# Kernel optimization log

Hardware: AMD Instinct MI355X
Metric: run time of the kernel (lower is better)

The kernel has to match this reference:

```python
import jax, jax.numpy as jnp
import numpy as np
import math

D_MODEL = 1024
NHEAD = 16
D_K = D_MODEL // NHEAD
SEQ = 2048
BATCH = 2


def setup_inputs() -> dict:
    key = jax.random.key(0)
    ks = jax.random.split(key, 8)
    s = 1.0 / math.sqrt(D_MODEL)
    return {
        "q": jax.random.normal(ks[0], (SEQ, BATCH, D_MODEL), jnp.float32),
        "k": jax.random.normal(ks[1], (SEQ, BATCH, D_MODEL), jnp.float32),
        "v": jax.random.normal(ks[2], (SEQ, BATCH, D_MODEL), jnp.float32),
        "mask": jnp.zeros((1, 1, SEQ, SEQ), jnp.float32),
        "Wq": jax.random.normal(ks[3], (D_MODEL, D_MODEL), jnp.float32) * s,
        "bq": jnp.zeros((D_MODEL,), jnp.float32),
        "Wk": jax.random.normal(ks[4], (D_MODEL, D_MODEL), jnp.float32) * s,
        "bk": jnp.zeros((D_MODEL,), jnp.float32),
        "Wv": jax.random.normal(ks[5], (D_MODEL, D_MODEL), jnp.float32) * s,
        "bv": jnp.zeros((D_MODEL,), jnp.float32),
        "Wo": jax.random.normal(ks[6], (D_MODEL, D_MODEL), jnp.float32) * s,
        "bo": jnp.zeros((D_MODEL,), jnp.float32),
    }


def _split_heads(x):
    # (seq, batch, d_model) -> (batch, nhead, seq, d_k)
    S, B, _ = x.shape
    return x.reshape(S, B, NHEAD, D_K).transpose(1, 2, 0, 3)


def reference(q, k, v, mask, Wq, bq, Wk, bk, Wv, bv, Wo, bo):
    S, B, _ = q.shape
    qh = _split_heads(q @ Wq.T + bq)  # (B, H, S, Dk)
    kh = _split_heads(k @ Wk.T + bk)
    vh = _split_heads(v @ Wv.T + bv)
    scale = 1.0 / math.sqrt(D_K)
    scores = jnp.einsum("bhsd,bhtd->bhst", qh, kh) * scale + mask
    attn = jax.nn.softmax(scores, axis=-1)  # dropout is identity at inference
    out = jnp.einsum("bhst,bhtd->bhsd", attn, vh)  # (B, H, S, Dk)
    # combine heads -> (S, B, d_model), then output projection
    out = out.transpose(2, 0, 1, 3).reshape(S, B, D_MODEL)
    return out @ Wo.T + bo
```

## Files before the change

kernel.cpp:

```cpp
#include <hip/hip_runtime.h>


#define DEV static __device__ __forceinline__

typedef unsigned short u16;
typedef __attribute__((ext_vector_type(8))) short short8;
typedef __attribute__((ext_vector_type(4))) float f32x4;
typedef __attribute__((ext_vector_type(16))) float f32x16;
typedef __attribute__((ext_vector_type(4))) unsigned short ushort4v;
typedef __attribute__((ext_vector_type(4))) unsigned int uint4v;

#define SEQ   2048
#define BATCH 2
#define DM    1024
#define NH    16
#define DKH   64
#define MROWS (SEQ*BATCH)

DEV u16 f2bf(float f) {
  union { float f; unsigned int u; } v; v.f = f;
  unsigned int u = v.u;
  return (u16)((u + 0x7FFFu + ((u >> 16) & 1u)) >> 16);
}

DEV unsigned int cvtpk_bf16(float lo, float hi) {
  unsigned int r;
  asm("v_cvt_pk_bf16_f32 %0, %1, %2" : "=v"(r) : "v"(lo), "v"(hi));
  return r;
}

DEV void permswap(unsigned int& a, unsigned int& b) {
  asm volatile("v_permlane32_swap_b32 %0, %1" : "+v"(a), "+v"(b));
}

#if __has_builtin(__builtin_amdgcn_exp2f)
#define EXP2(x) __builtin_amdgcn_exp2f(x)
#else
#define EXP2(x) exp2f(x)
#endif

DEV void async16(const void* g, void* l) {
  __builtin_amdgcn_global_load_lds(
      (const __attribute__((address_space(1))) unsigned int*)g,
      (__attribute__((address_space(3))) unsigned int*)l, 16, 0, 0);
}

struct CvtArgs {
  const float* s[8];
  u16* d[8];
  int n[8];
  float scale[8];
  int* flag;
};

__global__ __launch_bounds__(256) void cvt_kernel(CvtArgs a) {
  const int t = blockIdx.y;
  const int n = a.n[t];
  const int stride = 1024 * 256 * 4;
  if (t == 7) {
    const float* __restrict__ m = a.s[7];
    int any = 0;
    for (int i = (blockIdx.x * 256 + threadIdx.x) * 4; i < n; i += stride) {
      f32x4 v = *(const f32x4*)&m[i];
      any |= (v[0] != 0.f); any |= (v[1] != 0.f);
      any |= (v[2] != 0.f); any |= (v[3] != 0.f);
    }
    if (any) atomicOr(a.flag, 1);
    return;
  }
  const float* __restrict__ s = a.s[t];
  u16* __restrict__ d = a.d[t];
  const float sc = a.scale[t];
  for (int i = (blockIdx.x * 256 + threadIdx.x) * 4; i < n; i += stride) {
    f32x4 f = *(const f32x4*)&s[i];
    ushort4v o;
    o[0] = f2bf(f[0] * sc); o[1] = f2bf(f[1] * sc);
    o[2] = f2bf(f[2] * sc); o[3] = f2bf(f[3] * sc);
    *(ushort4v*)&d[i] = o;
  }
}

template <int MT, int NT, typename OutT>
DEV void gemm_body(const u16* __restrict__ A,
                   const u16* __restrict__ W,
                   const float* __restrict__ bias, float bscale,
                   OutT* __restrict__ C,
                   u16* As, u16* Bs,
                   int M, int N, int K, int m0, int n0) {
  const int tid = threadIdx.x;
  const int lane = tid & 63;
  const int wid = tid >> 6;
  const int wr = wid >> 1, wc = wid & 1;
  const int sr = lane & 15, g = lane >> 4;

  f32x4 acc[MT][NT] = {};

  const int arow = tid >> 3;
  const int acol = (tid & 7) * 8;
  const size_t abase = (size_t)(m0 + arow) * K + acol;
  const size_t bbase = (size_t)(n0 + arow) * K + acol;

  for (int kt = 0; kt < K; kt += 64) {
#pragma unroll
    for (int j = 0; j < MT; ++j)
      async16(A + abase + (size_t)j * 32 * K + kt, (char*)As + j * 4096 + wid * 1024);
#pragma unroll
    for (int j = 0; j < NT; ++j)
      async16(W + bbase + (size_t)j * 32 * K + kt, (char*)Bs + j * 4096 + wid * 1024);
    __syncthreads();
#pragma unroll
    for (int kk = 0; kk < 2; ++kk) {
      short8 af[MT], bf[NT];
#pragma unroll
      for (int mt = 0; mt < MT; ++mt)
        af[mt] = *(const short8*)&As[(wr * MT * 16 + mt * 16 + sr) * 64 + kk * 32 + g * 8];
#pragma unroll
      for (int nt = 0; nt < NT; ++nt)
        bf[nt] = *(const short8*)&Bs[(wc * NT * 16 + nt * 16 + sr) * 64 + kk * 32 + g * 8];
#pragma unroll
      for (int mt = 0; mt < MT; ++mt)
#pragma unroll
        for (int nt = 0; nt < NT; ++nt)
          acc[mt][nt] = __builtin_amdgcn_mfma_f32_16x16x32_bf16(af[mt], bf[nt], acc[mt][nt], 0, 0, 0);
    }
    __syncthreads();
  }

#pragma unroll
  for (int nt = 0; nt < NT; ++nt) {
    const int col = n0 + wc * NT * 16 + nt * 16 + sr;
    const float bv = bias[col] * bscale;
#pragma unroll
    for (int mt = 0; mt < MT; ++mt) {
#pragma unroll
      for (int r = 0; r < 4; ++r) {
        const int row = m0 + wr * MT * 16 + mt * 16 + g * 4 + r;
        const float val = acc[mt][nt][r] + bv;
        if constexpr (sizeof(OutT) == 2)
          C[(size_t)row * N + col] = f2bf(val);
        else
          C[(size_t)row * N + col] = val;
      }
    }
  }
}

struct GemmPtrs {
  const u16* A[3];
  const u16* W[3];
  const float* bias[3];
  float bscale[3];
  u16* C[3];
};

__global__ __launch_bounds__(256) void gemm_qkv_kernel(GemmPtrs p, int M, int N, int K) {
  __shared__ u16 As[64 * 64];
  __shared__ u16 Bs[128 * 64];
  const int z = blockIdx.z;
  const int fl = blockIdx.x + 64 * blockIdx.y;
  const int virt = (fl & 7) * 64 + (fl >> 3);
  const int mb = virt >> 3, nb = virt & 7;
  gemm_body<2, 4, u16>(p.A[z], p.W[z], p.bias[z], p.bscale[z], p.C[z], As, Bs,
                       M, N, K, mb * 64, nb * 128);
}

__global__ __launch_bounds__(256) void gemm_f32_kernel(const u16* __restrict__ A,
                                                       const u16* __restrict__ W,
                                                       const float* __restrict__ bias,
                                                       float* __restrict__ C,
                                                       int M, int N, int K) {
  __shared__ u16 As[64 * 64];
  __shared__ u16 Bs[128 * 64];
  const int fl = blockIdx.x + 64 * blockIdx.y;
  const int virt = (fl & 7) * 64 + (fl >> 3);
  const int mb = virt >> 3, nb = virt & 7;
  gemm_body<2, 4, float>(A, W, bias, 1.0f, C, As, Bs, M, N, K,
                         mb * 64, nb * 128);
}

__global__ __launch_bounds__(256) void vtrans_kernel(const u16* __restrict__ Vh,
                                                     u16* __restrict__ VT) {
  __shared__ u16 tl[4096];
  const int tid = threadIdx.x;
  const int w = tid >> 6;
  const int t0 = blockIdx.x * 64;
  const int bh = blockIdx.y;
  const int b = bh >> 4, h = bh & 15;
  const int str = tid >> 3;
  const int scc = (tid & 7) * 8;
#pragma unroll
  for (int it = 0; it < 2; ++it)
    async16(Vh + (size_t)((t0 + str + it * 32) * 2 + b) * 1024 + h * 64 + scc,
            (char*)tl + it * 4096 + w * 1024);
  __syncthreads();
  const int dk = tid >> 2;
  const int t4 = (tid & 3) * 16;
  short8 ov[2];
#pragma unroll
  for (int half = 0; half < 2; ++half)
#pragma unroll
    for (int j = 0; j < 8; ++j)
      ov[half][j] = (short)tl[(t4 + half * 8 + j) * 64 + dk];
  u16* dst = VT + (size_t)(bh * 64 + dk) * 2048 + t0 + t4;
  *(short8*)dst = ov[0];
  *(short8*)(dst + 8) = ov[1];
}

__global__ __launch_bounds__(256, 2) void attn8_kernel(const u16* __restrict__ Q,
                                                       const u16* __restrict__ K,
                                                       const u16* __restrict__ VT,
                                                       const float* __restrict__ mask,
                                                       const int* __restrict__ maskflag,
                                                       u16* __restrict__ O) {
  __shared__ u16 Kl[2][2][4096];
  __shared__ u16 Vl[2][2][4096];

  const int tid = threadIdx.x;
  const int lane = tid & 63;
  const int w = tid >> 6;
  const int ln = lane & 31;
  const int hi = lane >> 5;
  const int sw = (ln & 7) << 4;

  const int flat = blockIdx.x;
  const int virt = ((flat & 7) << 6) | (flat >> 3);
  const int qi = virt & 15;
  const int bh = virt >> 4;
  const int q0 = qi * 128 + w * 32;
  const int b = bh >> 4, h = bh & 15;
  const int usemask = *maskflag;

  const u16* Qb = Q + b * DM + h * DKH;
  const u16* Kb = K + b * DM + h * DKH;
  const u16* VTb = VT + (size_t)bh * 64 * 2048;

  short8 aq[4];
#pragma unroll
  for (int ks = 0; ks < 4; ++ks)
    aq[ks] = *(const short8*)&Qb[(size_t)(q0 + ln) * 2048 + ks * 16 + hi * 8];

  f32x16 acc[2] = {};
  float l_ = 0.f;
  const float L2E = 1.44269504088896f;

  const int strow = tid >> 3;
  const int scb = (((tid & 7) * 16) ^ ((strow & 7) << 4)) >> 1;

  auto STAGE = [&](int nb, int t0n) {
#pragma unroll
    for (int st = 0; st < 2; ++st)
#pragma unroll
      for (int it = 0; it < 2; ++it) {
        async16(Kb + (size_t)(t0n + st * 64 + strow + it * 32) * 2048 + scb,
                (char*)&Kl[nb][st][0] + it * 4096 + w * 1024);
        async16(VTb + (size_t)(strow + it * 32) * 2048 + t0n + st * 64 + scb,
                (char*)&Vl[nb][st][0] + it * 4096 + w * 1024);
      }
  };

  STAGE(0, 0);
  __syncthreads();
  int cur = 0;

  for (int tp = 0; tp < SEQ; tp += 128) {
    if (tp + 128 < SEQ) STAGE(cur ^ 1, tp + 128);

#pragma unroll
    for (int st = 0; st < 2; ++st) {
      const int t0 = tp + st * 64;

      short8 kf[2][4];
#pragma unroll
      for (int tb = 0; tb < 2; ++tb)
#pragma unroll
        for (int ks = 0; ks < 4; ++ks)
          kf[tb][ks] = *(const short8*)((const char*)&Kl[cur][st][0] +
                                        (tb * 32 + ln) * 128 + ((ks * 32 + hi * 16) ^ sw));

      f32x16 sc[2] = {};
      __builtin_amdgcn_s_setprio(1);
#pragma unroll
      for (int tb = 0; tb < 2; ++tb)
#pragma unroll
        for (int ks = 0; ks < 4; ++ks)
          sc[tb] = __builtin_amdgcn_mfma_f32_32x32x16_bf16(kf[tb][ks], aq[ks], sc[tb], 0, 0, 0);
      __builtin_amdgcn_s_setprio(0);

      short8 vf[2][4];
#pragma unroll
      for (int db = 0; db < 2; ++db)
#pragma unroll
        for (int ks = 0; ks < 4; ++ks)
          vf[db][ks] = *(const short8*)((const char*)&Vl[cur][st][0] +
                                        (db * 32 + ln) * 128 + ((ks * 32 + hi * 16) ^ sw));

      short8 pa[4];
      float rs = 0.f;
#pragma unroll
      for (int tb = 0; tb < 2; ++tb) {
        float p[16];
#pragma unroll
        for (int r = 0; r < 16; ++r) {
          float xv = sc[tb][r];
          if (usemask)
            xv = __builtin_fmaf(
                mask[(size_t)(q0 + ln) * SEQ + t0 + tb * 32 + (r & 3) + 8 * (r >> 2) + 4 * hi],
                L2E, xv);
          p[r] = EXP2(xv);
          rs += p[r];
        }
#pragma unroll
        for (int ksl = 0; ksl < 2; ++ksl) {
          unsigned int c0 = cvtpk_bf16(p[8 * ksl + 0], p[8 * ksl + 1]);
          unsigned int c1 = cvtpk_bf16(p[8 * ksl + 2], p[8 * ksl + 3]);
          unsigned int c4 = cvtpk_bf16(p[8 * ksl + 4], p[8 * ksl + 5]);
          unsigned int c5 = cvtpk_bf16(p[8 * ksl + 6], p[8 * ksl + 7]);
          permswap(c0, c4);
          permswap(c1, c5);
          union { uint4v u; short8 s; } cc;
          cc.u[0] = c0; cc.u[1] = c1; cc.u[2] = c4; cc.u[3] = c5;
          pa[tb * 2 + ksl] = cc.s;
        }
      }
      l_ += rs;

      __builtin_amdgcn_s_setprio(1);
#pragma unroll
      for (int ks = 0; ks < 4; ++ks)
#pragma unroll
        for (int db = 0; db < 2; ++db)
          acc[db] = __builtin_amdgcn_mfma_f32_32x32x16_bf16(pa[ks], vf[db][ks], acc[db], 0, 0, 0);
      __builtin_amdgcn_s_setprio(0);
    }

    __syncthreads();
    cur ^= 1;
  }

  l_ += __shfl_xor(l_, 32);
  const float linv = 1.f / l_;
  float lb[16];
#pragma unroll
  for (int r = 0; r < 16; ++r)
    lb[r] = __shfl(linv, (r & 3) + 8 * (r >> 2) + 4 * hi);
  const size_t obase = (size_t)b * DM + h * DKH;
#pragma unroll
  for (int db = 0; db < 2; ++db)
#pragma unroll
    for (int r = 0; r < 16; ++r) {
      const int q = q0 + (r & 3) + 8 * (r >> 2) + 4 * hi;
      O[(size_t)q * 2048 + obase + db * 32 + ln] = f2bf(acc[db][r] * lb[r]);
    }
}

extern "C" void kernel_launch(void* const* d_in, const int* in_sizes, int n_in,
                              void* d_out, int out_size, void* d_ws, size_t ws_size,
                              hipStream_t stream) {
  const float* q = (const float*)d_in[0];
  const float* k = (const float*)d_in[1];
  const float* v = (const float*)d_in[2];
  const float* msk = (const float*)d_in[3];
  const float* Wq = (const float*)d_in[4];
  const float* bq = (const float*)d_in[5];
  const float* Wk = (const float*)d_in[6];
  const float* bk = (const float*)d_in[7];
  const float* Wv = (const float*)d_in[8];
  const float* bv = (const float*)d_in[9];
  const float* Wo = (const float*)d_in[10];
  const float* bo = (const float*)d_in[11];
  float* out = (float*)d_out;

  char* ws = (char*)d_ws;
  const size_t SZX = (size_t)MROWS * DM * 2;
  const size_t SZW = (size_t)DM * DM * 2;
  u16* qb  = (u16*)(ws + 0 * SZX);
  u16* kb  = (u16*)(ws + 1 * SZX);
  u16* vb  = (u16*)(ws + 2 * SZX);
  u16* Wqb = (u16*)(ws + 3 * SZX + 0 * SZW);
  u16* Wkb = (u16*)(ws + 3 * SZX + 1 * SZW);
  u16* Wvb = (u16*)(ws + 3 * SZX + 2 * SZW);
  u16* Wob = (u16*)(ws + 3 * SZX + 3 * SZW);
  u16* Qh  = (u16*)(ws + 3 * SZX + 4 * SZW + 0 * SZX);
  u16* Kh  = (u16*)(ws + 3 * SZX + 4 * SZW + 1 * SZX);
  u16* Vh  = (u16*)(ws + 3 * SZX + 4 * SZW + 2 * SZX);
  u16* AO  = (u16*)(ws + 3 * SZX + 4 * SZW + 3 * SZX);
  int* flag = (int*)(ws + 7 * SZX + 4 * SZW);
  u16* VTg = qb;

  hipMemsetAsync(flag, 0, 4, stream);

  const float QS = 0.125f * 1.44269504088896f;

  CvtArgs ca;
  ca.s[0] = q;  ca.d[0] = qb;  ca.n[0] = MROWS * DM; ca.scale[0] = 1.f;
  ca.s[1] = k;  ca.d[1] = kb;  ca.n[1] = MROWS * DM; ca.scale[1] = 1.f;
  ca.s[2] = v;  ca.d[2] = vb;  ca.n[2] = MROWS * DM; ca.scale[2] = 1.f;
  ca.s[3] = Wq; ca.d[3] = Wqb; ca.n[3] = DM * DM;    ca.scale[3] = QS;
  ca.s[4] = Wk; ca.d[4] = Wkb; ca.n[4] = DM * DM;    ca.scale[4] = 1.f;
  ca.s[5] = Wv; ca.d[5] = Wvb; ca.n[5] = DM * DM;    ca.scale[5] = 1.f;
  ca.s[6] = Wo; ca.d[6] = Wob; ca.n[6] = DM * DM;    ca.scale[6] = 1.f;
  ca.s[7] = msk; ca.d[7] = nullptr; ca.n[7] = SEQ * SEQ; ca.scale[7] = 1.f;
  ca.flag = flag;
  cvt_kernel<<<dim3(1024, 8, 1), 256, 0, stream>>>(ca);

  GemmPtrs gp;
  gp.A[0] = qb; gp.W[0] = Wqb; gp.bias[0] = bq; gp.bscale[0] = QS;  gp.C[0] = Qh;
  gp.A[1] = kb; gp.W[1] = Wkb; gp.bias[1] = bk; gp.bscale[1] = 1.f; gp.C[1] = Kh;
  gp.A[2] = vb; gp.W[2] = Wvb; gp.bias[2] = bv; gp.bscale[2] = 1.f; gp.C[2] = Vh;
  gemm_qkv_kernel<<<dim3(64, 8, 3), 256, 0, stream>>>(gp, MROWS, DM, DM);

  vtrans_kernel<<<dim3(32, 32, 1), 256, 0, stream>>>(Vh, VTg);

  attn8_kernel<<<dim3(512, 1, 1), 256, 0, stream>>>(Qh, Kh, VTg, msk, flag, AO);

  gemm_f32_kernel<<<dim3(64, 8, 1), 256, 0, stream>>>(AO, Wob, bo, out, MROWS, DM, DM);
}
```

Before: 147.4 us.

## Fuse fp32-to-bf16 activation conversion into QKV GEMM and retile output GEMM

The QKV projection now loads the fp32 q/k/v activations straight into shared memory and converts them to bf16 while building the MFMA fragments. This removes the separate conversion pass over the three activation tensors and its bf16 round trip through memory. The cost is twice the shared-memory footprint and global traffic for the A tile, plus conversion ALU work that is repeated in every N-block. The output projection GEMM also moves to 64x64 tiles with twice as many blocks, trading per-block reuse for more parallelism.

```diff
diff --git a/kernel.cpp b/kernel.cpp
--- a/kernel.cpp
+++ b/kernel.cpp
@@ -57,8 +57,8 @@
   const int t = blockIdx.y;
   const int n = a.n[t];
   const int stride = 1024 * 256 * 4;
-  if (t == 7) {
-    const float* __restrict__ m = a.s[7];
+  if (a.d[t] == nullptr) {
+    const float* __restrict__ m = a.s[t];
     int any = 0;
     for (int i = (blockIdx.x * 256 + threadIdx.x) * 4; i < n; i += stride) {
       f32x4 v = *(const f32x4*)&m[i];
@@ -80,88 +80,90 @@
   }
 }
 
-template <int MT, int NT, typename OutT>
-DEV void gemm_body(const u16* __restrict__ A,
-                   const u16* __restrict__ W,
-                   const float* __restrict__ bias, float bscale,
-                   OutT* __restrict__ C,
-                   u16* As, u16* Bs,
-                   int M, int N, int K, int m0, int n0) {
+struct QkvArgs {
+  const float* A[3];
+  const u16* W[3];
+  const float* bias[3];
+  float bscale[3];
+  u16* C[3];
+};
+
+__global__ __launch_bounds__(256) void gemm_qkvf_kernel(QkvArgs p, int M, int N, int K) {
+  __shared__ float Asf[64 * 64];
+  __shared__ u16 Bs[128 * 64];
+  const int z = blockIdx.z;
+  const float* __restrict__ A = p.A[z];
+  const u16* __restrict__ W = p.W[z];
+  const int fl = blockIdx.x + 64 * blockIdx.y;
+  const int virt = (fl & 7) * 64 + (fl >> 3);
+  const int mb = virt >> 3, nb = virt & 7;
+  const int m0 = mb * 64, n0 = nb * 128;
+
   const int tid = threadIdx.x;
   const int lane = tid & 63;
   const int wid = tid >> 6;
   const int wr = wid >> 1, wc = wid & 1;
   const int sr = lane & 15, g = lane >> 4;
 
-  f32x4 acc[MT][NT] = {};
-
-  const int arow = tid >> 3;
-  const int acol = (tid & 7) * 8;
-  const size_t abase = (size_t)(m0 + arow) * K + acol;
-  const size_t bbase = (size_t)(n0 + arow) * K + acol;
+  f32x4 acc[2][4] = {};
+
+  const int arow_a = tid >> 4;
+  const int acol_a = (tid & 15) * 4;
+  const int arow_b = tid >> 3;
+  const int acol_b = (tid & 7) * 8;
 
   for (int kt = 0; kt < K; kt += 64) {
 #pragma unroll
-    for (int j = 0; j < MT; ++j)
-      async16(A + abase + (size_t)j * 32 * K + kt, (char*)As + j * 4096 + wid * 1024);
-#pragma unroll
-    for (int j = 0; j < NT; ++j)
-      async16(W + bbase + (size_t)j * 32 * K + kt, (char*)Bs + j * 4096 + wid * 1024);
+    for (int it = 0; it < 4; ++it)
+      async16(A + (size_t)(m0 + it * 16 + arow_a) * K + kt + acol_a,
+              (char*)Asf + it * 4096 + wid * 1024);
+#pragma unroll
+    for (int j = 0; j < 4; ++j)
+      async16(W + (size_t)(n0 + j * 32 + arow_b) * K + kt + acol_b,
+              (char*)Bs + j * 4096 + wid * 1024);
     __syncthreads();
 #pragma unroll
     for (int kk = 0; kk < 2; ++kk) {
-      short8 af[MT], bf[NT];
-#pragma unroll
-      for (int mt = 0; mt < MT; ++mt)
-        af[mt] = *(const short8*)&As[(wr * MT * 16 + mt * 16 + sr) * 64 + kk * 32 + g * 8];
-#pragma unroll
-      for (int nt = 0; nt < NT; ++nt)
-        bf[nt] = *(const short8*)&Bs[(wc * NT * 16 + nt * 16 + sr) * 64 + kk * 32 + g * 8];
-#pragma unroll
-      for (int mt = 0; mt < MT; ++mt)
-#pragma unroll
-        for (int nt = 0; nt < NT; ++nt)
+      short8 af[2], bf[4];
+#pragma unroll
+      for (int mt = 0; mt < 2; ++mt) {
+        const float* ap = &Asf[(wr * 32 + mt * 16 + sr) * 64 + kk * 32 + g * 8];
+        f32x4 a0 = *(const f32x4*)ap;
+        f32x4 a1 = *(const f32x4*)(ap + 4);
+        union { uint4v u; short8 s; } ca_;
+        ca_.u[0] = cvtpk_bf16(a0[0], a0[1]);
+        ca_.u[1] = cvtpk_bf16(a0[2], a0[3]);
+        ca_.u[2] = cvtpk_bf16(a1[0], a1[1]);
+        ca_.u[3] = cvtpk_bf16(a1[2], a1[3]);
+        af[mt] = ca_.s;
+      }
+#pragma unroll
+      for (int nt = 0; nt < 4; ++nt)
+        bf[nt] = *(const short8*)&Bs[(wc * 64 + nt * 16 + sr) * 64 + kk * 32 + g * 8];
+#pragma unroll
+      for (int mt = 0; mt < 2; ++mt)
+#pragma unroll
+        for (int nt = 0; nt < 4; ++nt)
           acc[mt][nt] = __builtin_amdgcn_mfma_f32_16x16x32_bf16(af[mt], bf[nt], acc[mt][nt], 0, 0, 0);
     }
     __syncthreads();
   }
 
-#pragma unroll
-  for (int nt = 0; nt < NT; ++nt) {
-    const int col = n0 + wc * NT * 16 + nt * 16 + sr;
+  const float* __restrict__ bias = p.bias[z];
+  const float bscale = p.bscale[z];
+  u16* __restrict__ C = p.C[z];
+#pragma unroll
+  for (int nt = 0; nt < 4; ++nt) {
+    const int col = n0 + wc * 64 + nt * 16 + sr;
     const float bv = bias[col] * bscale;
 #pragma unroll
-    for (int mt = 0; mt < MT; ++mt) {
+    for (int mt = 0; mt < 2; ++mt)
 #pragma unroll
       for (int r = 0; r < 4; ++r) {
-        const int row = m0 + wr * MT * 16 + mt * 16 + g * 4 + r;
-        const float val = acc[mt][nt][r] + bv;
-        if constexpr (sizeof(OutT) == 2)
-          C[(size_t)row * N + col] = f2bf(val);
-        else
-          C[(size_t)row * N + col] = val;
+        const int row = m0 + wr * 32 + mt * 16 + g * 4 + r;
+        C[(size_t)row * N + col] = f2bf(acc[mt][nt][r] + bv);
       }
-    }
-  }
-}
-
-struct GemmPtrs {
-  const u16* A[3];
-  const u16* W[3];
-  const float* bias[3];
-  float bscale[3];
-  u16* C[3];
-};
-
-__global__ __launch_bounds__(256) void gemm_qkv_kernel(GemmPtrs p, int M, int N, int K) {
-  __shared__ u16 As[64 * 64];
-  __shared__ u16 Bs[128 * 64];
-  const int z = blockIdx.z;
-  const int fl = blockIdx.x + 64 * blockIdx.y;
-  const int virt = (fl & 7) * 64 + (fl >> 3);
-  const int mb = virt >> 3, nb = virt & 7;
-  gemm_body<2, 4, u16>(p.A[z], p.W[z], p.bias[z], p.bscale[z], p.C[z], As, Bs,
-                       M, N, K, mb * 64, nb * 128);
+  }
 }
 
 __global__ __launch_bounds__(256) void gemm_f32_kernel(const u16* __restrict__ A,
@@ -170,12 +172,62 @@
                                                        float* __restrict__ C,
                                                        int M, int N, int K) {
   __shared__ u16 As[64 * 64];
-  __shared__ u16 Bs[128 * 64];
+  __shared__ u16 Bs[64 * 64];
   const int fl = blockIdx.x + 64 * blockIdx.y;
-  const int virt = (fl & 7) * 64 + (fl >> 3);
-  const int mb = virt >> 3, nb = virt & 7;
-  gemm_body<2, 4, float>(A, W, bias, 1.0f, C, As, Bs, M, N, K,
-                         mb * 64, nb * 128);
+  const int virt = (fl & 7) * 128 + (fl >> 3);
+  const int mb = virt >> 4, nb = virt & 15;
+  const int m0 = mb * 64, n0 = nb * 64;
+
+  const int tid = threadIdx.x;
+  const int lane = tid & 63;
+  const int wid = tid >> 6;
+  const int wr = wid >> 1, wc = wid & 1;
+  const int sr = lane & 15, g = lane >> 4;
+
+  f32x4 acc[2][2] = {};
+
+  const int arow = tid >> 3;
+  const int acol = (tid & 7) * 8;
+  const size_t abase = (size_t)(m0 + arow) * K + acol;
+  const size_t bbase = (size_t)(n0 + arow) * K + acol;
+
+  for (int kt = 0; kt < K; kt += 64) {
+#pragma unroll
+    for (int j = 0; j < 2; ++j) {
+      async16(A + abase + (size_t)j * 32 * K + kt, (char*)As + j * 4096 + wid * 1024);
+      async16(W + bbase + (size_t)j * 32 * K + kt, (char*)Bs + j * 4096 + wid * 1024);
+    }
+    __syncthreads();
+#pragma unroll
+    for (int kk = 0; kk < 2; ++kk) {
+      short8 af[2], bf[2];
+#pragma unroll
+      for (int mt = 0; mt < 2; ++mt)
+        af[mt] = *(const short8*)&As[(wr * 32 + mt * 16 + sr) * 64 + kk * 32 + g * 8];
+#pragma unroll
+      for (int nt = 0; nt < 2; ++nt)
+        bf[nt] = *(const short8*)&Bs[(wc * 32 + nt * 16 + sr) * 64 + kk * 32 + g * 8];
+#pragma unroll
+      for (int mt = 0; mt < 2; ++mt)
+#pragma unroll
+        for (int nt = 0; nt < 2; ++nt)
+          acc[mt][nt] = __builtin_amdgcn_mfma_f32_16x16x32_bf16(af[mt], bf[nt], acc[mt][nt], 0, 0, 0);
+    }
+    __syncthreads();
+  }
+
+#pragma unroll
+  for (int nt = 0; nt < 2; ++nt) {
+    const int col = n0 + wc * 32 + nt * 16 + sr;
+    const float bv = bias[col];
+#pragma unroll
+    for (int mt = 0; mt < 2; ++mt)
+#pragma unroll
+      for (int r = 0; r < 4; ++r) {
+        const int row = m0 + wr * 32 + mt * 16 + g * 4 + r;
+        C[(size_t)row * N + col] = acc[mt][nt][r] + bv;
+      }
+  }
 }
 
 __global__ __launch_bounds__(256) void vtrans_kernel(const u16* __restrict__ Vh,
@@ -373,9 +425,6 @@
   char* ws = (char*)d_ws;
   const size_t SZX = (size_t)MROWS * DM * 2;
   const size_t SZW = (size_t)DM * DM * 2;
-  u16* qb  = (u16*)(ws + 0 * SZX);
-  u16* kb  = (u16*)(ws + 1 * SZX);
-  u16* vb  = (u16*)(ws + 2 * SZX);
   u16* Wqb = (u16*)(ws + 3 * SZX + 0 * SZW);
   u16* Wkb = (u16*)(ws + 3 * SZX + 1 * SZW);
   u16* Wvb = (u16*)(ws + 3 * SZX + 2 * SZW);
@@ -385,33 +434,30 @@
   u16* Vh  = (u16*)(ws + 3 * SZX + 4 * SZW + 2 * SZX);
   u16* AO  = (u16*)(ws + 3 * SZX + 4 * SZW + 3 * SZX);
   int* flag = (int*)(ws + 7 * SZX + 4 * SZW);
-  u16* VTg = qb;
+  u16* VTg = (u16*)(ws + 0 * SZX);
 
   hipMemsetAsync(flag, 0, 4, stream);
 
   const float QS = 0.125f * 1.44269504088896f;
 
-  CvtArgs ca;
-  ca.s[0] = q;  ca.d[0] = qb;  ca.n[0] = MROWS * DM; ca.scale[0] = 1.f;
-  ca.s[1] = k;  ca.d[1] = kb;  ca.n[1] = MROWS * DM; ca.scale[1] = 1.f;
-  ca.s[2] = v;  ca.d[2] = vb;  ca.n[2] = MROWS * DM; ca.scale[2] = 1.f;
-  ca.s[3] = Wq; ca.d[3] = Wqb; ca.n[3] = DM * DM;    ca.scale[3] = QS;
-  ca.s[4] = Wk; ca.d[4] = Wkb; ca.n[4] = DM * DM;    ca.scale[4] = 1.f;
-  ca.s[5] = Wv; ca.d[5] = Wvb; ca.n[5] = DM * DM;    ca.scale[5] = 1.f;
-  ca.s[6] = Wo; ca.d[6] = Wob; ca.n[6] = DM * DM;    ca.scale[6] = 1.f;
-  ca.s[7] = msk; ca.d[7] = nullptr; ca.n[7] = SEQ * SEQ; ca.scale[7] = 1.f;
+  CvtArgs ca = {};
+  ca.s[0] = Wq; ca.d[0] = Wqb; ca.n[0] = DM * DM;    ca.scale[0] = QS;
+  ca.s[1] = Wk; ca.d[1] = Wkb; ca.n[1] = DM * DM;    ca.scale[1] = 1.f;
+  ca.s[2] = Wv; ca.d[2] = Wvb; ca.n[2] = DM * DM;    ca.scale[2] = 1.f;
+  ca.s[3] = Wo; ca.d[3] = Wob; ca.n[3] = DM * DM;    ca.scale[3] = 1.f;
+  ca.s[4] = msk; ca.d[4] = nullptr; ca.n[4] = SEQ * SEQ; ca.scale[4] = 1.f;
   ca.flag = flag;
-  cvt_kernel<<<dim3(1024, 8, 1), 256, 0, stream>>>(ca);
-
-  GemmPtrs gp;
-  gp.A[0] = qb; gp.W[0] = Wqb; gp.bias[0] = bq; gp.bscale[0] = QS;  gp.C[0] = Qh;
-  gp.A[1] = kb; gp.W[1] = Wkb; gp.bias[1] = bk; gp.bscale[1] = 1.f; gp.C[1] = Kh;
-  gp.A[2] = vb; gp.W[2] = Wvb; gp.bias[2] = bv; gp.bscale[2] = 1.f; gp.C[2] = Vh;
-  gemm_qkv_kernel<<<dim3(64, 8, 3), 256, 0, stream>>>(gp, MROWS, DM, DM);
+  cvt_kernel<<<dim3(1024, 5, 1), 256, 0, stream>>>(ca);
+
+  QkvArgs gp;
+  gp.A[0] = q; gp.W[0] = Wqb; gp.bias[0] = bq; gp.bscale[0] = QS;  gp.C[0] = Qh;
+  gp.A[1] = k; gp.W[1] = Wkb; gp.bias[1] = bk; gp.bscale[1] = 1.f; gp.C[1] = Kh;
+  gp.A[2] = v; gp.W[2] = Wvb; gp.bias[2] = bv; gp.bscale[2] = 1.f; gp.C[2] = Vh;
+  gemm_qkvf_kernel<<<dim3(64, 8, 3), 256, 0, stream>>>(gp, MROWS, DM, DM);
 
   vtrans_kernel<<<dim3(32, 32, 1), 256, 0, stream>>>(Vh, VTg);
 
   attn8_kernel<<<dim3(512, 1, 1), 256, 0, stream>>>(Qh, Kh, VTg, msk, flag, AO);
 
-  gemm_f32_kernel<<<dim3(64, 8, 1), 256, 0, stream>>>(AO, Wob, bo, out, MROWS, DM, DM);
-}
+  gemm_f32_kernel<<<dim3(64, 16, 1), 256, 0, stream>>>(AO, Wob, bo, out, MROWS, DM, DM);
+}
```

Result: slower. 163.3 us (+10.8%).
